# Optimization experiments

Hardware: AMD Instinct MI355X
Metric: run time of the kernel (lower is better)

## Reference

```python
import jax, jax.numpy as jnp
import numpy as np

B, C, H, W = 4, 256, 64, 64

def setup_inputs() -> dict:
    key = jax.random.key(0)
    k1, k2, k3, k4, k5, k6 = jax.random.split(key, 6)
    input_1 = jax.random.normal(k1, (B, C, H, W), dtype=jnp.float32)
    input_2 = jax.random.normal(k2, (B, C, H, W), dtype=jnp.float32)
    W_e = jax.random.normal(k3, (C, C), dtype=jnp.float32) * 0.02   # linear_e weight [out,in]
    gate_w = jax.random.normal(k4, (C,), dtype=jnp.float32) * 0.01  # Conv2d(c,1,1) weight squeezed
    W1 = jax.random.normal(k5, (C, 2 * C), dtype=jnp.float32) * 0.01  # final_conv_1 1x1 weight [out,in]
    W2 = jax.random.normal(k6, (C, 2 * C), dtype=jnp.float32) * 0.01  # final_conv_2
    return {"input_1": input_1, "input_2": input_2, "W_e": W_e,
            "gate_w": gate_w, "W1": W1, "W2": W2}

def reference(input_1, input_2, W_e, gate_w, W1, W2):
    b, c, h, w = input_1.shape
    hw = h * w
    ex = input_1.reshape(b, c, hw)   # exemplar_flat (b,c,n)
    q = input_2.reshape(b, c, hw)    # query_flat    (b,c,m)
    # linear_e on exemplar^T: (b,n,c) @ W_e^T -> (b,n,c)
    ec = jnp.einsum('bcn,dc->bnd', ex, W_e)
    # correlation A: (b,n,m)
    A = jnp.einsum('bnd,bdm->bnm', ec, q)
    A1 = jax.nn.softmax(A, axis=1)                       # softmax over exemplar pixels n
    Bmat = jax.nn.softmax(jnp.swapaxes(A, 1, 2), axis=1)  # (b,m,n), softmax over query pixels m
    query_att = jnp.einsum('bcn,bnm->bcm', ex, A1).reshape(b, c, h, w)
    exemplar_att = jnp.einsum('bcm,bmn->bcn', q, Bmat).reshape(b, c, h, w)
    # gate: 1x1 conv to 1 channel + sigmoid + elementwise mul
    m1 = jax.nn.sigmoid(jnp.einsum('bchw,c->bhw', exemplar_att, gate_w))[:, None]
    m2 = jax.nn.sigmoid(jnp.einsum('bchw,c->bhw', query_att, gate_w))[:, None]
    att1 = jnp.concatenate([exemplar_att * m1, input_1], axis=1)  # (b,2c,h,w)
    att2 = jnp.concatenate([query_att * m2, input_2], axis=1)
    out1 = jnp.einsum('bkhw,ok->bohw', att1, W1)
    out2 = jnp.einsum('bkhw,ok->bohw', att2, W2)
    return out1, out2
```

## Files before the change

kernel.cpp:

```cpp
#include <hip/hip_runtime.h>
#include <cstdint>
#include <cstddef>

#define BATCH 4
#define CCH   256
#define HW    4096
#define NM    4096

typedef __attribute__((ext_vector_type(8))) short s16x8;
typedef __attribute__((ext_vector_type(4))) float f32x4;

__device__ __forceinline__ short f2bf(float f) {
    unsigned u = __float_as_uint(f);
    u += 0x7FFFu + ((u >> 16) & 1u);
    return (short)(u >> 16);
}
__device__ __forceinline__ float bf2f(short s) {
    return __uint_as_float(((unsigned)(unsigned short)s) << 16);
}

__device__ __forceinline__ void gload16(const void* g, void* l) {
    __builtin_amdgcn_global_load_lds(
        (const __attribute__((address_space(1))) unsigned int*)g,
        (__attribute__((address_space(3))) unsigned int*)l, 16, 0, 0);
}

__global__ __launch_bounds__(256) void k_cast(const float* __restrict__ s,
                                              short* __restrict__ d, int n) {
    int i = (blockIdx.x * 256 + threadIdx.x) * 4;
    if (i + 3 < n) {
        float4 v = *(const float4*)&s[i];
        *(short4*)&d[i] = make_short4(f2bf(v.x), f2bf(v.y), f2bf(v.z), f2bf(v.w));
    }
}

__global__ __launch_bounds__(256) void k_prep(const float* __restrict__ in1,
                                              const float* __restrict__ in2,
                                              short* __restrict__ X16,
                                              short* __restrict__ Q16,
                                              short* __restrict__ Xt16,
                                              short* __restrict__ Qt16) {
    __shared__ short S[64][72];
    int t = threadIdx.x;
    int p0 = blockIdx.x * 64, c0 = blockIdx.y * 64;
    int z = blockIdx.z;
    int b = z >> 1, which = z & 1;
    const float* src = (which ? in2 : in1) + (size_t)b * CCH * HW;
    short* direct = (which ? Q16 : X16) + (size_t)b * CCH * HW;
    short* trans  = (which ? Qt16 : Xt16) + (size_t)b * HW * CCH;
    int tx = t & 15, ty = t >> 4;
#pragma unroll
    for (int i = 0; i < 4; ++i) {
        int c = ty + i * 16;
        float4 v = *(const float4*)&src[(size_t)(c0 + c) * HW + p0 + tx * 4];
        short4 h = make_short4(f2bf(v.x), f2bf(v.y), f2bf(v.z), f2bf(v.w));
        *(short4*)&direct[(size_t)(c0 + c) * HW + p0 + tx * 4] = h;
        S[tx * 4 + 0][c] = h.x;
        S[tx * 4 + 1][c] = h.y;
        S[tx * 4 + 2][c] = h.z;
        S[tx * 4 + 3][c] = h.w;
    }
    __syncthreads();
#pragma unroll
    for (int i = 0; i < 4; ++i) {
        int p = ty + i * 16;
        short4 v = *(const short4*)&S[p][tx * 4];
        *(short4*)&trans[(size_t)(p0 + p) * CCH + c0 + tx * 4] = v;
    }
}

__global__ __launch_bounds__(256) void k_E_mfma(const short* __restrict__ Xt16,
                                                const short* __restrict__ We16,
                                                short* __restrict__ E16n) {
    __shared__ short As[128 * 72];
    __shared__ short Bs[128 * 72];
    int t = threadIdx.x;
    int d0 = blockIdx.x * 128, n0 = blockIdx.y * 128, b = blockIdx.z;
    const short* Xb = Xt16 + (size_t)b * HW * CCH;
    short* Eb = E16n + (size_t)b * HW * CCH;
    int lm = t & 15, q = (t >> 4) & 3, w = t >> 6;
    int wr = (w >> 1) * 64, wc = (w & 1) * 64;
    f32x4 acc[4][4];
#pragma unroll
    for (int i = 0; i < 4; ++i)
#pragma unroll
        for (int j = 0; j < 4; ++j) acc[i][j] = (f32x4){0.f, 0.f, 0.f, 0.f};

    for (int k0 = 0; k0 < CCH; k0 += 64) {
#pragma unroll
        for (int u = 0; u < 4; ++u) {
            int chunk = t + u * 256;
            int row = chunk >> 3, off = (chunk & 7) * 8;
            *(float4*)&As[row * 72 + off] =
                *(const float4*)&Xb[(size_t)(n0 + row) * CCH + k0 + off];
            *(float4*)&Bs[row * 72 + off] =
                *(const float4*)&We16[(size_t)(d0 + row) * CCH + k0 + off];
        }
        __syncthreads();
#pragma unroll
        for (int kk = 0; kk < 2; ++kk) {
            s16x8 af[4], bfr[4];
#pragma unroll
            for (int i = 0; i < 4; ++i)
                af[i] = *(const s16x8*)&As[(wr + i * 16 + lm) * 72 + kk * 32 + q * 8];
#pragma unroll
            for (int j = 0; j < 4; ++j)
                bfr[j] = *(const s16x8*)&Bs[(wc + j * 16 + lm) * 72 + kk * 32 + q * 8];
#pragma unroll
            for (int i = 0; i < 4; ++i)
#pragma unroll
                for (int j = 0; j < 4; ++j)
                    acc[i][j] = __builtin_amdgcn_mfma_f32_16x16x32_bf16(
                        af[i], bfr[j], acc[i][j], 0, 0, 0);
        }
        __syncthreads();
    }
#pragma unroll
    for (int i = 0; i < 4; ++i)
#pragma unroll
        for (int r = 0; r < 4; ++r) {
            size_t base = (size_t)(n0 + wr + i * 16 + q * 4 + r) * CCH;
#pragma unroll
            for (int j = 0; j < 4; ++j)
                Eb[base + d0 + wc + j * 16 + lm] = f2bf(acc[i][j][r]);
        }
}

__global__ __launch_bounds__(512, 2) void k_fused(const short* __restrict__ E16n,
                                                  const short* __restrict__ Qt16,
                                                  const short* __restrict__ Q16,
                                                  const short* __restrict__ X16,
                                                  const float* __restrict__ gw,
                                                  short* __restrict__ eattT,
                                                  short* __restrict__ qattT,
                                                  float* __restrict__ m1v,
                                                  float* __restrict__ m2v) {
    __shared__ short AcS[128 * 256];
    __shared__ short Ps[128 * 264];
    __shared__ float rs[128];
    __shared__ float grs[8 * 128];

    int t = threadIdx.x;
    int gid = blockIdx.x;
    int unit = gid & 7;
    int b = unit >> 1, which = unit & 1;
    int r0 = (gid >> 3) * 128;

    const short* Ar = (which ? Qt16 : E16n) + (size_t)b * HW * CCH;
    const short* Ac = (which ? E16n : Qt16) + (size_t)b * HW * CCH;
    const short* V  = (which ? X16  : Q16 ) + (size_t)b * CCH * HW;
    short* Out = (which ? qattT : eattT) + (size_t)b * HW * CCH;
    float* mdst = (which ? m2v : m1v) + (size_t)b * HW;

    int lm = t & 15, q = (t >> 4) & 3, w = t >> 6;
    int lane = t & 63;
    int cq = w * 32;

    float gwv[2];
#pragma unroll
    for (int j = 0; j < 2; ++j) gwv[j] = gw[cq + j * 16 + lm];

    s16x8 af[8];
#pragma unroll
    for (int kk = 0; kk < 8; ++kk)
        af[kk] = *(const s16x8*)&Ar[(size_t)(r0 + w * 16 + lm) * CCH + kk * 32 + q * 8];

    {
        const char* AcB = (const char*)Ac;
#pragma unroll
        for (int c = 0; c < 8; ++c) {
            int Lb = (w * 8 + c) << 10;
            int L = Lb + lane * 16;
            int col = L >> 9;
            int soff = (col << 9) | ((L & 511) ^ ((col & 7) << 4));
            gload16(AcB + soff, (char*)AcS + Lb);
        }
    }
    __syncthreads();

    f32x4 oacc[8][2];
    float rsum[4];
#pragma unroll
    for (int i = 0; i < 8; ++i)
#pragma unroll
        for (int j = 0; j < 2; ++j) oacc[i][j] = (f32x4){0.f, 0.f, 0.f, 0.f};
#pragma unroll
    for (int r = 0; r < 4; ++r) rsum[r] = 0.f;

    for (int col0 = 0; col0 < NM; col0 += 128) {
        s16x8 vf[4][2];
#pragma unroll
        for (int km = 0; km < 4; ++km)
#pragma unroll
            for (int j = 0; j < 2; ++j)
                vf[km][j] = *(const s16x8*)&V[(size_t)(cq + j * 16 + lm) * HW +
                                              col0 + km * 32 + q * 8];

        f32x4 sacc[8];
#pragma unroll
        for (int j = 0; j < 8; ++j) sacc[j] = (f32x4){0.f, 0.f, 0.f, 0.f};
#pragma unroll
        for (int kk = 0; kk < 8; ++kk) {
            int swk = ((kk * 64 + q * 16) ^ ((lm & 7) << 4)) >> 1;
            s16x8 bf[8];
#pragma unroll
            for (int j = 0; j < 8; ++j)
                bf[j] = *(const s16x8*)&AcS[(j * 16 + lm) * 256 + swk];
#pragma unroll
            for (int j = 0; j < 8; ++j)
                sacc[j] = __builtin_amdgcn_mfma_f32_16x16x32_bf16(
                    af[kk], bf[j], sacc[j], 0, 0, 0);
        }
#pragma unroll
        for (int j = 0; j < 8; ++j)
#pragma unroll
            for (int r = 0; r < 4; ++r) {
                float v = bf2f(f2bf(__expf(sacc[j][r])));
                rsum[r] += v;
                sacc[j][r] = v;
            }
#pragma unroll
        for (int j = 0; j < 8; ++j)
#pragma unroll
            for (int r = 0; r < 4; ++r)
                Ps[(w * 16 + q * 4 + r) * 264 + j * 16 + lm] =
                    (short)(__float_as_uint(sacc[j][r]) >> 16);
        __syncthreads();

        if (col0 + 128 < NM) {
            const char* AcB = (const char*)(Ac + (size_t)(col0 + 128) * CCH);
#pragma unroll
            for (int c = 0; c < 8; ++c) {
                int Lb = (w * 8 + c) << 10;
                int L = Lb + lane * 16;
                int col = L >> 9;
                int soff = (col << 9) | ((L & 511) ^ ((col & 7) << 4));
                gload16(AcB + soff, (char*)AcS + Lb);
            }
        }

#pragma unroll
        for (int km = 0; km < 4; ++km) {
            s16x8 pf[8];
#pragma unroll
            for (int i = 0; i < 8; ++i)
                pf[i] = *(const s16x8*)&Ps[(i * 16 + lm) * 264 + km * 32 + q * 8];
#pragma unroll
            for (int i = 0; i < 8; ++i)
#pragma unroll
                for (int j = 0; j < 2; ++j)
                    oacc[i][j] = __builtin_amdgcn_mfma_f32_16x16x32_bf16(
                        pf[i], vf[km][j], oacc[i][j], 0, 0, 0);
        }
        __syncthreads();
    }

#pragma unroll
    for (int r = 0; r < 4; ++r) {
        float s = rsum[r];
        s += __shfl_xor(s, 1, 64);
        s += __shfl_xor(s, 2, 64);
        s += __shfl_xor(s, 4, 64);
        s += __shfl_xor(s, 8, 64);
        if (lm == 0) rs[w * 16 + q * 4 + r] = s;
    }
    __syncthreads();

    float gacc[8][4];
#pragma unroll
    for (int i = 0; i < 8; ++i)
#pragma unroll
        for (int r = 0; r < 4; ++r) {
            int row = i * 16 + q * 4 + r;
            float inv = 1.f / rs[row];
            size_t base = (size_t)(r0 + row) * CCH;
            float ga = 0.f;
#pragma unroll
            for (int j = 0; j < 2; ++j) {
                short h = f2bf(oacc[i][j][r] * inv);
                Out[base + cq + j * 16 + lm] = h;
                ga = fmaf(bf2f(h), gwv[j], ga);
            }
            gacc[i][r] = ga;
        }
#pragma unroll
    for (int i = 0; i < 8; ++i)
#pragma unroll
        for (int r = 0; r < 4; ++r) {
            float s = gacc[i][r];
            s += __shfl_xor(s, 1, 64);
            s += __shfl_xor(s, 2, 64);
            s += __shfl_xor(s, 4, 64);
            s += __shfl_xor(s, 8, 64);
            if (lm == 0) grs[w * 128 + i * 16 + q * 4 + r] = s;
        }
    __syncthreads();
    if (t < 128) {
        float g = 0.f;
#pragma unroll
        for (int ww = 0; ww < 8; ++ww) g += grs[ww * 128 + t];
        mdst[r0 + t] = 1.f / (1.f + __expf(-g));
    }
}

__global__ __launch_bounds__(256) void k_final(const short* __restrict__ W16_1,
                                               const short* __restrict__ W16_2,
                                               const short* __restrict__ eattT,
                                               const short* __restrict__ qattT,
                                               const short* __restrict__ Xt16,
                                               const short* __restrict__ Qt16,
                                               const float* __restrict__ m1v,
                                               const float* __restrict__ m2v,
                                               float* __restrict__ outbase) {
    __shared__ short As[128 * 40];
    __shared__ short Bs[64 * 40];
    int t = threadIdx.x;
    int zz = blockIdx.z;
    int half = zz >> 2, b = zz & 3;
    const short* W16 = half ? W16_2 : W16_1;
    const short* attT = (half ? qattT : eattT);
    const short* inT  = (half ? Qt16 : Xt16);
    const float* gate = half ? m2v : m1v;
    float* outp = outbase + (size_t)half * BATCH * CCH * HW;
    int p0 = blockIdx.x * 64, o0 = blockIdx.y * 128;
    const short* Tb0 = attT + (size_t)b * HW * CCH;
    const short* Tb1 = inT + (size_t)b * HW * CCH;
    int lm = t & 15, q = (t >> 4) & 3, w = t >> 6;
    int wr = (w >> 1) * 64, wc = (w & 1) * 32;
    f32x4 acc[2][4][2];
#pragma unroll
    for (int ph = 0; ph < 2; ++ph)
#pragma unroll
        for (int i = 0; i < 4; ++i)
#pragma unroll
            for (int j = 0; j < 2; ++j) acc[ph][i][j] = (f32x4){0.f, 0.f, 0.f, 0.f};

    int brow = t >> 2, boff = (t & 3) * 8;
    for (int ph = 0; ph < 2; ++ph) {
        const short* Tb = ph ? Tb1 : Tb0;
        for (int k0 = 0; k0 < CCH; k0 += 32) {
#pragma unroll
            for (int u = 0; u < 2; ++u) {
                int chunk = t + u * 256;
                int row = chunk >> 2, off = (chunk & 3) * 8;
                *(float4*)&As[row * 40 + off] =
                    *(const float4*)&W16[(size_t)(o0 + row) * 512 + ph * 256 + k0 + off];
            }
            *(float4*)&Bs[brow * 40 + boff] =
                *(const float4*)&Tb[(size_t)(p0 + brow) * CCH + k0 + boff];
            __syncthreads();
            s16x8 af[4], bfr[2];
#pragma unroll
            for (int i = 0; i < 4; ++i)
                af[i] = *(const s16x8*)&As[(wr + i * 16 + lm) * 40 + q * 8];
#pragma unroll
            for (int j = 0; j < 2; ++j)
                bfr[j] = *(const s16x8*)&Bs[(wc + j * 16 + lm) * 40 + q * 8];
#pragma unroll
            for (int i = 0; i < 4; ++i)
#pragma unroll
                for (int j = 0; j < 2; ++j)
                    acc[ph][i][j] = __builtin_amdgcn_mfma_f32_16x16x32_bf16(
                        af[i], bfr[j], acc[ph][i][j], 0, 0, 0);
            __syncthreads();
        }
    }
#pragma unroll
    for (int j = 0; j < 2; ++j) {
        int p = p0 + wc + j * 16 + lm;
        float gv = gate[(size_t)b * HW + p];
#pragma unroll
        for (int i = 0; i < 4; ++i)
#pragma unroll
            for (int r = 0; r < 4; ++r) {
                int o = o0 + wr + i * 16 + q * 4 + r;
                outp[((size_t)b * CCH + o) * HW + p] =
                    acc[0][i][j][r] * gv + acc[1][i][j][r];
            }
    }
}

extern "C" void kernel_launch(void* const* d_in, const int* in_sizes, int n_in,
                              void* d_out, int out_size, void* d_ws, size_t ws_size,
                              hipStream_t stream) {
    (void)in_sizes; (void)n_in; (void)out_size; (void)ws_size;
    const float* in1 = (const float*)d_in[0];
    const float* in2 = (const float*)d_in[1];
    const float* We  = (const float*)d_in[2];
    const float* gw  = (const float*)d_in[3];
    const float* W1  = (const float*)d_in[4];
    const float* W2  = (const float*)d_in[5];
    float* out = (float*)d_out;
    char* ws = (char*)d_ws;

    const size_t SB = (size_t)BATCH * CCH * HW * 2;
    const size_t WB = (size_t)CCH * 2 * CCH * 2;
    const size_t EB = (size_t)CCH * CCH * 2;
    const size_t VB = (size_t)BATCH * NM * 4;

    size_t off = 0;
    auto alloc = [&](size_t bytes) {
        char* p = ws + off;
        off += (bytes + 255) & ~(size_t)255;
        return p;
    };
    short* W16_1 = (short*)alloc(WB);
    short* W16_2 = (short*)alloc(WB);
    short* We16  = (short*)alloc(EB);
    short* Xt16  = (short*)alloc(SB);
    short* Qt16  = (short*)alloc(SB);
    short* E16n  = (short*)alloc(SB);
    short* eattT = (short*)alloc(SB);
    short* qattT = (short*)alloc(SB);
    short* X16   = (short*)alloc(SB);
    short* Q16   = (short*)alloc(SB);
    float* m1v   = (float*)alloc(VB);
    float* m2v   = (float*)alloc(VB);

    const int nW = CCH * 2 * CCH;
    const int nWe = CCH * CCH;

    k_cast<<<dim3(nW / 1024), 256, 0, stream>>>(W1, W16_1, nW);
    k_cast<<<dim3(nW / 1024), 256, 0, stream>>>(W2, W16_2, nW);
    k_cast<<<dim3(nWe / 1024), 256, 0, stream>>>(We, We16, nWe);
    k_prep<<<dim3(HW / 64, CCH / 64, 8), 256, 0, stream>>>(in1, in2, X16, Q16,
                                                           Xt16, Qt16);

    k_E_mfma<<<dim3(2, 32, BATCH), 256, 0, stream>>>(Xt16, We16, E16n);

    k_fused<<<dim3((HW / 128) * 8), 512, 0, stream>>>(E16n, Qt16, Q16, X16, gw,
                                                      eattT, qattT, m1v, m2v);

    k_final<<<dim3(64, 2, 8), 256, 0, stream>>>(W16_1, W16_2, eattT, qattT,
                                                Xt16, Qt16, m1v, m2v, out);
}
```

Baseline: 295.7 us.

## Retile fused attention warps into 2D grids to cut LDS fragment reloads

Warps in the fused attention kernel now work on 2D sub-tiles instead of full-width strips. The score GEMM uses a 2x4 grid of 32 rows by 64 columns, and the P·V GEMM uses a 2x4 grid of 64 rows by 64 channels. Each warp reads half as many B/P fragments from LDS and reuses each over more MFMAs. Row sums are now combined from two column halves and gate partials from four channel groups. The P buffer shrinks to a 128x132 layout, and half of the V fragment loads move after the barrier to overlap with compute. In exchange, per-thread register use rises (A fragments and V fragments double), which risks spills or lower occupancy.

Measured after the change: 388.2 us. 31.3% more time.

```diff
diff --git a/kernel.cpp b/kernel.cpp
--- a/kernel.cpp
+++ b/kernel.cpp
@@ -136,9 +136,9 @@
                                                   float* __restrict__ m1v,
                                                   float* __restrict__ m2v) {
     __shared__ short AcS[128 * 256];
-    __shared__ short Ps[128 * 264];
-    __shared__ float rs[128];
-    __shared__ float grs[8 * 128];
+    __shared__ short Ps[128 * 132];
+    __shared__ float rs[2 * 128];
+    __shared__ float grs[4 * 128];
 
     int t = threadIdx.x;
     int gid = blockIdx.x;
@@ -154,16 +154,21 @@
 
     int lm = t & 15, q = (t >> 4) & 3, w = t >> 6;
     int lane = t & 63;
-    int cq = w * 32;
-
-    float gwv[2];
-#pragma unroll
-    for (int j = 0; j < 2; ++j) gwv[j] = gw[cq + j * 16 + lm];
-
-    s16x8 af[8];
-#pragma unroll
-    for (int kk = 0; kk < 8; ++kk)
-        af[kk] = *(const s16x8*)&Ar[(size_t)(r0 + w * 16 + lm) * CCH + kk * 32 + q * 8];
+    int wr = w >> 1, wc = w & 1;
+    int wrp = w >> 2, wcp = w & 3;
+    int cq = wcp * 64;
+
+    float gwv[4];
+#pragma unroll
+    for (int j = 0; j < 4; ++j) gwv[j] = gw[cq + j * 16 + lm];
+
+    s16x8 af[2][8];
+#pragma unroll
+    for (int i = 0; i < 2; ++i)
+#pragma unroll
+        for (int kk = 0; kk < 8; ++kk)
+            af[i][kk] = *(const s16x8*)&Ar[(size_t)(r0 + wr * 32 + i * 16 + lm) * CCH +
+                                           kk * 32 + q * 8];
 
     {
         const char* AcB = (const char*)Ac;
@@ -178,54 +183,71 @@
     }
     __syncthreads();
 
-    f32x4 oacc[8][2];
-    float rsum[4];
-#pragma unroll
-    for (int i = 0; i < 8; ++i)
-#pragma unroll
-        for (int j = 0; j < 2; ++j) oacc[i][j] = (f32x4){0.f, 0.f, 0.f, 0.f};
-#pragma unroll
-    for (int r = 0; r < 4; ++r) rsum[r] = 0.f;
+    f32x4 oacc[4][4];
+    float rsum[2][4];
+#pragma unroll
+    for (int i = 0; i < 4; ++i)
+#pragma unroll
+        for (int j = 0; j < 4; ++j) oacc[i][j] = (f32x4){0.f, 0.f, 0.f, 0.f};
+#pragma unroll
+    for (int i = 0; i < 2; ++i)
+#pragma unroll
+        for (int r = 0; r < 4; ++r) rsum[i][r] = 0.f;
 
     for (int col0 = 0; col0 < NM; col0 += 128) {
-        s16x8 vf[4][2];
-#pragma unroll
-        for (int km = 0; km < 4; ++km)
-#pragma unroll
-            for (int j = 0; j < 2; ++j)
+        s16x8 vf[4][4];
+#pragma unroll
+        for (int km = 0; km < 2; ++km)
+#pragma unroll
+            for (int j = 0; j < 4; ++j)
                 vf[km][j] = *(const s16x8*)&V[(size_t)(cq + j * 16 + lm) * HW +
                                               col0 + km * 32 + q * 8];
 
-        f32x4 sacc[8];
-#pragma unroll
-        for (int j = 0; j < 8; ++j) sacc[j] = (f32x4){0.f, 0.f, 0.f, 0.f};
+        f32x4 sacc[2][4];
+#pragma unroll
+        for (int i = 0; i < 2; ++i)
+#pragma unroll
+            for (int j = 0; j < 4; ++j) sacc[i][j] = (f32x4){0.f, 0.f, 0.f, 0.f};
 #pragma unroll
         for (int kk = 0; kk < 8; ++kk) {
             int swk = ((kk * 64 + q * 16) ^ ((lm & 7) << 4)) >> 1;
-            s16x8 bf[8];
-#pragma unroll
-            for (int j = 0; j < 8; ++j)
-                bf[j] = *(const s16x8*)&AcS[(j * 16 + lm) * 256 + swk];
-#pragma unroll
-            for (int j = 0; j < 8; ++j)
-                sacc[j] = __builtin_amdgcn_mfma_f32_16x16x32_bf16(
-                    af[kk], bf[j], sacc[j], 0, 0, 0);
-        }
-#pragma unroll
-        for (int j = 0; j < 8; ++j)
-#pragma unroll
-            for (int r = 0; r < 4; ++r) {
-                float v = bf2f(f2bf(__expf(sacc[j][r])));
-                rsum[r] += v;
-                sacc[j][r] = v;
-            }
-#pragma unroll
-        for (int j = 0; j < 8; ++j)
-#pragma unroll
-            for (int r = 0; r < 4; ++r)
-                Ps[(w * 16 + q * 4 + r) * 264 + j * 16 + lm] =
-                    (short)(__float_as_uint(sacc[j][r]) >> 16);
+            s16x8 bf[4];
+#pragma unroll
+            for (int j = 0; j < 4; ++j)
+                bf[j] = *(const s16x8*)&AcS[(wc * 64 + j * 16 + lm) * 256 + swk];
+#pragma unroll
+            for (int i = 0; i < 2; ++i)
+#pragma unroll
+                for (int j = 0; j < 4; ++j)
+                    sacc[i][j] = __builtin_amdgcn_mfma_f32_16x16x32_bf16(
+                        af[i][kk], bf[j], sacc[i][j], 0, 0, 0);
+        }
+#pragma unroll
+        for (int i = 0; i < 2; ++i)
+#pragma unroll
+            for (int j = 0; j < 4; ++j)
+#pragma unroll
+                for (int r = 0; r < 4; ++r) {
+                    float v = bf2f(f2bf(__expf(sacc[i][j][r])));
+                    rsum[i][r] += v;
+                    sacc[i][j][r] = v;
+                }
+#pragma unroll
+        for (int i = 0; i < 2; ++i)
+#pragma unroll
+            for (int j = 0; j < 4; ++j)
+#pragma unroll
+                for (int r = 0; r < 4; ++r)
+                    Ps[(wr * 32 + i * 16 + q * 4 + r) * 132 + wc * 64 + j * 16 + lm] =
+                        (short)(__float_as_uint(sacc[i][j][r]) >> 16);
         __syncthreads();
+
+#pragma unroll
+        for (int km = 2; km < 4; ++km)
+#pragma unroll
+            for (int j = 0; j < 4; ++j)
+                vf[km][j] = *(const s16x8*)&V[(size_t)(cq + j * 16 + lm) * HW +
+                                              col0 + km * 32 + q * 8];
 
         if (col0 + 128 < NM) {
             const char* AcB = (const char*)(Ac + (size_t)(col0 + 128) * CCH);
@@ -241,14 +263,15 @@
 
 #pragma unroll
         for (int km = 0; km < 4; ++km) {
-            s16x8 pf[8];
-#pragma unroll
-            for (int i = 0; i < 8; ++i)
-                pf[i] = *(const s16x8*)&Ps[(i * 16 + lm) * 264 + km * 32 + q * 8];
-#pragma unroll
-            for (int i = 0; i < 8; ++i)
-#pragma unroll
-                for (int j = 0; j < 2; ++j)
+            s16x8 pf[4];
+#pragma unroll
+            for (int i = 0; i < 4; ++i)
+                pf[i] = *(const s16x8*)&Ps[(wrp * 64 + i * 16 + lm) * 132 +
+                                           km * 32 + q * 8];
+#pragma unroll
+            for (int i = 0; i < 4; ++i)
+#pragma unroll
+                for (int j = 0; j < 4; ++j)
                     oacc[i][j] = __builtin_amdgcn_mfma_f32_16x16x32_bf16(
                         pf[i], vf[km][j], oacc[i][j], 0, 0, 0);
         }
@@ -256,27 +279,29 @@
     }
 
 #pragma unroll
-    for (int r = 0; r < 4; ++r) {
-        float s = rsum[r];
-        s += __shfl_xor(s, 1, 64);
-        s += __shfl_xor(s, 2, 64);
-        s += __shfl_xor(s, 4, 64);
-        s += __shfl_xor(s, 8, 64);
-        if (lm == 0) rs[w * 16 + q * 4 + r] = s;
-    }
+    for (int i = 0; i < 2; ++i)
+#pragma unroll
+        for (int r = 0; r < 4; ++r) {
+            float s = rsum[i][r];
+            s += __shfl_xor(s, 1, 64);
+            s += __shfl_xor(s, 2, 64);
+            s += __shfl_xor(s, 4, 64);
+            s += __shfl_xor(s, 8, 64);
+            if (lm == 0) rs[wc * 128 + wr * 32 + i * 16 + q * 4 + r] = s;
+        }
     __syncthreads();
 
-    float gacc[8][4];
-#pragma unroll
-    for (int i = 0; i < 8; ++i)
+    float gacc[4][4];
+#pragma unroll
+    for (int i = 0; i < 4; ++i)
 #pragma unroll
         for (int r = 0; r < 4; ++r) {
-            int row = i * 16 + q * 4 + r;
-            float inv = 1.f / rs[row];
+            int row = wrp * 64 + i * 16 + q * 4 + r;
+            float inv = 1.f / (rs[row] + rs[128 + row]);
             size_t base = (size_t)(r0 + row) * CCH;
             float ga = 0.f;
 #pragma unroll
-            for (int j = 0; j < 2; ++j) {
+            for (int j = 0; j < 4; ++j) {
                 short h = f2bf(oacc[i][j][r] * inv);
                 Out[base + cq + j * 16 + lm] = h;
                 ga = fmaf(bf2f(h), gwv[j], ga);
@@ -284,7 +309,7 @@
             gacc[i][r] = ga;
         }
 #pragma unroll
-    for (int i = 0; i < 8; ++i)
+    for (int i = 0; i < 4; ++i)
 #pragma unroll
         for (int r = 0; r < 4; ++r) {
             float s = gacc[i][r];
@@ -292,13 +317,11 @@
             s += __shfl_xor(s, 2, 64);
             s += __shfl_xor(s, 4, 64);
             s += __shfl_xor(s, 8, 64);
-            if (lm == 0) grs[w * 128 + i * 16 + q * 4 + r] = s;
+            if (lm == 0) grs[wcp * 128 + wrp * 64 + i * 16 + q * 4 + r] = s;
         }
     __syncthreads();
     if (t < 128) {
-        float g = 0.f;
-#pragma unroll
-        for (int ww = 0; ww < 8; ++ww) g += grs[ww * 128 + t];
+        float g = grs[t] + grs[128 + t] + grs[256 + t] + grs[384 + t];
         mdst[r0 + t] = 1.f / (1.f + __expf(-g));
     }
 }
```
